# Optimization experiments

Hardware: AMD Instinct MI355X
Metric: run time of the kernel (lower is better)

Reference implementation:

```python
import jax, jax.numpy as jnp
import numpy as np

N_MET = 100_000
N_RXN = 50_000
E_SUB = 2_000_000
E_ALL = 4_000_000
MSG_DIM = 16
HIDDEN = 32


def setup_inputs() -> dict:
    key = jax.random.key(0)
    ks = jax.random.split(key, 16)
    x_met = jax.random.normal(ks[0], (N_MET,), dtype=jnp.float32)
    sto_sub = jax.random.uniform(ks[1], (E_SUB,), dtype=jnp.float32, minval=0.0, maxval=1.0)
    sto_all = jax.random.normal(ks[2], (E_ALL,), dtype=jnp.float32)
    met_sub = jax.random.randint(ks[3], (E_SUB,), 0, N_MET)
    rxn_sub = jax.random.randint(ks[4], (E_SUB,), 0, N_RXN)
    met_all = jax.random.randint(ks[5], (E_ALL,), 0, N_MET)
    rxn_all = jax.random.randint(ks[6], (E_ALL,), 0, N_RXN)
    # msg_mlp: Linear(2->HIDDEN), Tanh, Linear(HIDDEN->MSG_DIM)
    W1m = jax.random.normal(ks[7], (2, HIDDEN), jnp.float32) / np.sqrt(2.0)
    b1m = jnp.zeros((HIDDEN,), jnp.float32)
    W2m = jax.random.normal(ks[8], (HIDDEN, MSG_DIM), jnp.float32) / np.sqrt(HIDDEN)
    b2m = jnp.zeros((MSG_DIM,), jnp.float32)
    # rate_mlp: Linear(MSG_DIM->HIDDEN), Tanh, Linear(HIDDEN->1)
    W1r = jax.random.normal(ks[9], (MSG_DIM, HIDDEN), jnp.float32) / np.sqrt(MSG_DIM)
    b1r = jnp.zeros((HIDDEN,), jnp.float32)
    W2r = jax.random.normal(ks[10], (HIDDEN, 1), jnp.float32) / np.sqrt(HIDDEN)
    b2r = jnp.zeros((1,), jnp.float32)
    return {
        "x_met": x_met, "sto_sub": sto_sub, "sto_all": sto_all,
        "W1m": W1m, "b1m": b1m, "W2m": W2m, "b2m": b2m,
        "W1r": W1r, "b1r": b1r, "W2r": W2r, "b2r": b2r,
        "met_sub": met_sub, "rxn_sub": rxn_sub,
        "met_all": met_all, "rxn_all": rxn_all,
    }


def reference(x_met, sto_sub, sto_all, W1m, b1m, W2m, b2m, W1r, b1r, W2r, b2r,
              met_sub, rxn_sub, met_all, rxn_all):
    # gather substrate node features and build per-edge MLP input [E_sub, 2]
    msg_in = jnp.stack([x_met[met_sub], sto_sub], axis=-1)
    # msg MLP: tanh hidden, linear out -> [E_sub, MSG_DIM]
    msg = jnp.tanh(msg_in @ W1m + b1m) @ W2m + b2m
    # scatter-add messages into reactions -> [N_RXN, MSG_DIM]
    h_rxn = jax.ops.segment_sum(msg, rxn_sub, num_segments=N_RXN)
    # rate MLP + softplus -> per-reaction rate v [N_RXN]
    v = jax.nn.softplus((jnp.tanh(h_rxn @ W1r + b1r) @ W2r + b2r)[:, 0])
    # stoichiometric contributions scattered into metabolites -> dxdt [N_MET]
    contrib = sto_all * v[rxn_all]
    dxdt = jax.ops.segment_sum(contrib, met_all, num_segments=N_MET)
    return dxdt, v
```

## Files before the change

### kernel.cpp

```cpp
#include <hip/hip_runtime.h>

#define N_MET 100000
#define N_RXN 50000
#define E_SUB 2000000
#define E_ALL 4000000
#define MSG_DIM 16
#define HIDDEN 32

#define NBKT_A 391
#define NB_ALL 245
#define TILE_A 16384
#define SLOT_A 12288
#define NBKT_S 782
#define NB_SUB 245
#define TILE_S 8192
#define SLOT_S 4096
#define CHUNK_M 3072


__device__ __forceinline__ float fast_tanh(float x) {
    const float e = __expf(2.0f * x);
    return 1.0f - 2.0f * __builtin_amdgcn_rcpf(e + 1.0f);
}

__global__ __launch_bounds__(1024) void zero_cnt_kernel(
    int* __restrict__ gs, int* __restrict__ ga)
{
    const int t = threadIdx.x;
    for (int i = t; i < NBKT_S; i += 1024) gs[i] = 0;
    for (int i = t; i < NBKT_A; i += 1024) ga[i] = 0;
}


__global__ __launch_bounds__(1024) void scatter_bin_sub_kernel(
    const float* __restrict__ x_met, const float* __restrict__ sto_sub,
    const int* __restrict__ met_sub, const int* __restrict__ rxn_sub,
    int* __restrict__ gcnt, float2* __restrict__ pxs)
{
    __shared__ float2 se[TILE_S];
    __shared__ int cnt[NBKT_S];
    __shared__ int loff[NBKT_S + 1];
    __shared__ int roff[NBKT_S];
    const int t = threadIdx.x, bk = blockIdx.x;
    for (int i = t; i < NBKT_S; i += 1024) cnt[i] = 0;
    __syncthreads();

    const int e0 = bk * TILE_S;
    const int rem = min(TILE_S, E_SUB - e0);
    const int tb = 8 * t;
    float2 pay[8]; int meta[8];
    if (tb + 8 <= rem) {
        const int4 r01 = ((const int4*)(rxn_sub + e0))[2 * t];
        const int4 r23 = ((const int4*)(rxn_sub + e0))[2 * t + 1];
        const int4 m01 = ((const int4*)(met_sub + e0))[2 * t];
        const int4 m23 = ((const int4*)(met_sub + e0))[2 * t + 1];
        const float4 s01 = ((const float4*)(sto_sub + e0))[2 * t];
        const float4 s23 = ((const float4*)(sto_sub + e0))[2 * t + 1];
        const int rr[8] = {r01.x, r01.y, r01.z, r01.w, r23.x, r23.y, r23.z, r23.w};
        const int mm[8] = {m01.x, m01.y, m01.z, m01.w, m23.x, m23.y, m23.z, m23.w};
        const float ss[8] = {s01.x, s01.y, s01.z, s01.w, s23.x, s23.y, s23.z, s23.w};
#pragma unroll
        for (int k = 0; k < 8; ++k) {
            const int r = rr[k];
            const float x = x_met[mm[k]];
            const int sb = (__float_as_int(ss[k]) & ~63) | (r & 63);
            pay[k] = make_float2(x, __int_as_float(sb));
            const int q = r >> 6;
            meta[k] = (atomicAdd(&cnt[q], 1) << 10) | q;
        }
    } else {
#pragma unroll
        for (int k = 0; k < 8; ++k) {
            const int e = e0 + tb + k;
            if (e < E_SUB) {
                const int r = rxn_sub[e];
                const float x = x_met[met_sub[e]];
                const int sb = (__float_as_int(sto_sub[e]) & ~63) | (r & 63);
                pay[k] = make_float2(x, __int_as_float(sb));
                const int q = r >> 6;
                meta[k] = (atomicAdd(&cnt[q], 1) << 10) | q;
            } else meta[k] = -1;
        }
    }
    __syncthreads();

    if (t < 64) {
        int carry = 0;
        for (int bb = 0; bb < NBKT_S; bb += 64) {
            const int idx = bb + t;
            const int val = (idx < NBKT_S) ? cnt[idx] : 0;
            int x = val;
#pragma unroll
            for (int off = 1; off < 64; off <<= 1) {
                const int y = __shfl_up(x, off);
                if (t >= off) x += y;
            }
            if (idx < NBKT_S) loff[idx] = carry + x - val;
            carry += __shfl(x, 63);
        }
        if (t == 0) loff[NBKT_S] = carry;
    }
    __syncthreads();

#pragma unroll
    for (int k = 0; k < 8; ++k) {
        if (meta[k] >= 0)
            se[loff[meta[k] & 1023] + (meta[k] >> 10)] = pay[k];
    }
    for (int q = t; q < NBKT_S; q += 1024) {
        const int len = loff[q + 1] - loff[q];
        roff[q] = len ? atomicAdd(&gcnt[q], len) : 0;
    }
    __syncthreads();

    const int qw = t >> 4, ql = t & 15;
    for (int q = qw; q < NBKT_S; q += 64) {
        const int s = loff[q], len = loff[q + 1] - s;
        float2* d = pxs + (size_t)q * SLOT_S + roff[q];
        for (int i = ql; i < len; i += 16)
            d[i] = se[s + i];
    }
}

__global__ __launch_bounds__(512, 8) void bucket_msg_kernel(
    const float2* __restrict__ pxs, const int* __restrict__ gcnt,
    const float* __restrict__ W1m, const float* __restrict__ b1m,
    const float* __restrict__ W2m, const float* __restrict__ b2m,
    const float* __restrict__ W1r, const float* __restrict__ b1r,
    const float* __restrict__ W2r, const float* __restrict__ b2r,
    float* __restrict__ v)
{
    __shared__ float2 se[CHUNK_M];
    __shared__ float  sth[64 * 33];
    __shared__ int    cnt[64];
    __shared__ int    soff[65];
    __shared__ int    ccnt[64];
    __shared__ float  sW2m[HIDDEN * MSG_DIM];
    __shared__ float  sb2m[MSG_DIM];
    __shared__ float  sW1r[MSG_DIM * HIDDEN];
    __shared__ float  sb1r[HIDDEN];
    __shared__ float  sW2r[HIDDEN];
    __shared__ float  sb2r;
    float* const sh = (float*)se;

    const int t = threadIdx.x;
    const int w = t >> 6, l = t & 63;
    const int half = l >> 5, j = l & 31;

    for (int i = t; i < HIDDEN * MSG_DIM; i += 512) sW2m[i] = W2m[i];
    for (int i = t; i < MSG_DIM * HIDDEN; i += 512) sW1r[i] = W1r[i];
    if (t < MSG_DIM) sb2m[t] = b2m[t];
    if (t < HIDDEN) sb1r[t] = b1r[t];
    if (t >= 64 && t < 64 + HIDDEN) sW2r[t - 64] = W2r[t - 64];
    if (t == 128) sb2r = b2r[0];
    if (t < 64) ccnt[t] = 0;

    const float w1x = W1m[j];
    const float w1y = W1m[HIDDEN + j];
    const float w1b = b1m[j];

    const int b = blockIdx.x;
    const int beg = b * SLOT_S;
    const int end = beg + gcnt[b];

    float acc[4] = {0.0f, 0.0f, 0.0f, 0.0f};

    for (int cb = beg; cb < end; cb += CHUNK_M) {
        if (t < 64) cnt[t] = 0;
        __syncthreads();

        float2 pay[6];
        int meta[6];
#pragma unroll
        for (int k = 0; k < 6; ++k) {
            const int idx = cb + t + (k << 9);
            if (idx < end && t + (k << 9) < CHUNK_M) {
                const float2 pv = pxs[idx];
                const int r = __float_as_int(pv.y) & 63;
                meta[k] = (atomicAdd(&cnt[r], 1) << 6) | r;
                pay[k] = pv;
            } else meta[k] = -1;
        }
        __syncthreads();

        if (t < 64) {
            const int orig = cnt[t];
            int x = orig;
#pragma unroll
            for (int off = 1; off < 64; off <<= 1) {
                const int y = __shfl_up(x, off);
                if (t >= off) x += y;
            }
            soff[t] = x - orig;
            if (t == 63) soff[64] = x;
            ccnt[t] += orig;
        }
        __syncthreads();

#pragma unroll
        for (int k = 0; k < 6; ++k) {
            if (meta[k] >= 0)
                se[soff[meta[k] & 63] + (meta[k] >> 6)] = pay[k];
        }
        __syncthreads();

#pragma unroll
        for (int p = 0; p < 4; ++p) {
            const int q = (w << 3) + (p << 1) + half;
            const int rb = soff[q];
            const int rl = soff[q + 1] - rb;
            float a0 = 0.0f, a1 = 0.0f;
            int i = 0;
            for (; i + 2 <= rl; i += 2) {
                const float2 e0 = se[rb + i];
                const float2 e1 = se[rb + i + 1];
                a0 += fast_tanh(fmaf(e0.x, w1x, fmaf(e0.y, w1y, w1b)));
                a1 += fast_tanh(fmaf(e1.x, w1x, fmaf(e1.y, w1y, w1b)));
            }
            if (i < rl) {
                const float2 e0 = se[rb + i];
                a0 += fast_tanh(fmaf(e0.x, w1x, fmaf(e0.y, w1y, w1b)));
            }
            acc[p] += a0 + a1;
        }
        __syncthreads();
    }

#pragma unroll
    for (int p = 0; p < 4; ++p) {
        const int q = (w << 3) + (p << 1) + half;
        sth[q * 33 + j] = acc[p];
    }
    __syncthreads();

    {
        const int r = t & 63, g = (t >> 6) << 1;
        const float cntf = (float)ccnt[r];
        float h0 = cntf * sb2m[g + 0], h1 = cntf * sb2m[g + 1];
#pragma unroll 8
        for (int jj = 0; jj < HIDDEN; ++jj) {
            const float ts = sth[r * 33 + jj];
            h0 = fmaf(ts, sW2m[jj * MSG_DIM + g + 0], h0);
            h1 = fmaf(ts, sW2m[jj * MSG_DIM + g + 1], h1);
        }
        sh[r * 17 + g + 0] = h0;
        sh[r * 17 + g + 1] = h1;
    }
    __syncthreads();

    if (t < 64) {
        const int r = b * 64 + t;
        if (r < N_RXN) {
            float h[MSG_DIM];
#pragma unroll
            for (int d = 0; d < MSG_DIM; ++d) h[d] = sh[t * 17 + d];
            float acc2 = sb2r;
#pragma unroll 2
            for (int jj = 0; jj < HIDDEN; ++jj) {
                float z = sb1r[jj];
#pragma unroll
                for (int d = 0; d < MSG_DIM; ++d)
                    z = fmaf(h[d], sW1r[d * HIDDEN + jj], z);
                acc2 = fmaf(fast_tanh(z), sW2r[jj], acc2);
            }
            v[r] = fmaxf(acc2, 0.0f) + log1pf(expf(-fabsf(acc2)));
        }
    }
}


__global__ __launch_bounds__(1024) void scatter_bin_kernel(
    const float* __restrict__ sto_all, const float* __restrict__ v,
    const int* __restrict__ met_all, const int* __restrict__ rxn_all,
    int* __restrict__ gcntA, float* __restrict__ pc)
{
    __shared__ float sp[TILE_A];
    __shared__ int cnt[NBKT_A];
    __shared__ int loff[NBKT_A + 1];
    __shared__ int roff[NBKT_A];
    const int t = threadIdx.x, bk = blockIdx.x;
    for (int i = t; i < NBKT_A; i += 1024) cnt[i] = 0;
    __syncthreads();

    const int e0 = bk * TILE_A;
    const int rem = min(TILE_A, E_ALL - e0);
    const int tb = 16 * t;
    int meta[16];
    const bool full = (tb + 16 <= rem);
    if (full) {
#pragma unroll
        for (int kk = 0; kk < 4; ++kk) {
            const int4 m = ((const int4*)(met_all + e0))[4 * t + kk];
            meta[4 * kk + 0] = (atomicAdd(&cnt[m.x >> 8], 1) << 17) | m.x;
            meta[4 * kk + 1] = (atomicAdd(&cnt[m.y >> 8], 1) << 17) | m.y;
            meta[4 * kk + 2] = (atomicAdd(&cnt[m.z >> 8], 1) << 17) | m.z;
            meta[4 * kk + 3] = (atomicAdd(&cnt[m.w >> 8], 1) << 17) | m.w;
        }
    } else {
#pragma unroll
        for (int k = 0; k < 16; ++k) {
            const int e = e0 + tb + k;
            if (e < E_ALL) {
                const int m = met_all[e];
                meta[k] = (atomicAdd(&cnt[m >> 8], 1) << 17) | m;
            } else meta[k] = -1;
        }
    }
    __syncthreads();

    if (t < 64) {
        int carry = 0;
        for (int bb = 0; bb < NBKT_A; bb += 64) {
            const int idx = bb + t;
            const int val = (idx < NBKT_A) ? cnt[idx] : 0;
            int x = val;
#pragma unroll
            for (int off = 1; off < 64; off <<= 1) {
                const int y = __shfl_up(x, off);
                if (t >= off) x += y;
            }
            if (idx < NBKT_A) loff[idx] = carry + x - val;
            carry += __shfl(x, 63);
        }
        if (t == 0) loff[NBKT_A] = carry;
    }
    __syncthreads();

    for (int q = t; q < NBKT_A; q += 1024) {
        const int len = loff[q + 1] - loff[q];
        roff[q] = len ? atomicAdd(&gcntA[q], len) : 0;
    }

    if (full) {
#pragma unroll
        for (int kk = 0; kk < 4; ++kk) {
            const int4 r = ((const int4*)(rxn_all + e0))[4 * t + kk];
            const float4 s = ((const float4*)(sto_all + e0))[4 * t + kk];
            const int rr[4] = {r.x, r.y, r.z, r.w};
            const float ss[4] = {s.x, s.y, s.z, s.w};
#pragma unroll
            for (int u = 0; u < 4; ++u) {
                const int mt = meta[4 * kk + u];
                const int m = mt & 0x1FFFF;
                const float c = ss[u] * v[rr[u]];
                const int cb = (__float_as_int(c) & ~255) | (m & 255);
                sp[loff[m >> 8] + (mt >> 17)] = __int_as_float(cb);
            }
        }
    } else {
#pragma unroll
        for (int k = 0; k < 16; ++k) {
            const int e = e0 + tb + k;
            if (e < E_ALL) {
                const int mt = meta[k];
                const int m = mt & 0x1FFFF;
                const float c = sto_all[e] * v[rxn_all[e]];
                const int cb = (__float_as_int(c) & ~255) | (m & 255);
                sp[loff[m >> 8] + (mt >> 17)] = __int_as_float(cb);
            }
        }
    }
    __syncthreads();

    const int qw = t >> 4, ql = t & 15;
    for (int q = qw; q < NBKT_A; q += 64) {
        const int s = loff[q], len = loff[q + 1] - s;
        float* d = pc + (size_t)q * SLOT_A + roff[q];
        for (int i = ql; i < len; i += 16)
            d[i] = sp[s + i];
    }
}

__global__ __launch_bounds__(512) void bucket_accum_kernel(
    const float* __restrict__ pc, const int* __restrict__ gcntA,
    float* __restrict__ dxdt)
{
    __shared__ float acc[256];
    const int q = blockIdx.x, t = threadIdx.x;
    if (t < 256) acc[t] = 0.0f;
    __syncthreads();
    const float* s = pc + (size_t)q * SLOT_A;
    const int n = gcntA[q];
    const int n4 = n & ~3;
    for (int i = 4 * t; i < n4; i += 2048) {
        const float4 pv = *(const float4*)(s + i);
        atomicAdd(&acc[__float_as_int(pv.x) & 255], pv.x);
        atomicAdd(&acc[__float_as_int(pv.y) & 255], pv.y);
        atomicAdd(&acc[__float_as_int(pv.z) & 255], pv.z);
        atomicAdd(&acc[__float_as_int(pv.w) & 255], pv.w);
    }
    for (int i = n4 + t; i < n; i += 512) {
        const float pv = s[i];
        atomicAdd(&acc[__float_as_int(pv) & 255], pv);
    }
    __syncthreads();
    if (t < 256) {
        const int met = q * 256 + t;
        if (met < N_MET) dxdt[met] = acc[t];
    }
}

extern "C" void kernel_launch(void* const* d_in, const int* in_sizes, int n_in,
                              void* d_out, int out_size, void* d_ws, size_t ws_size,
                              hipStream_t stream) {
    const float* x_met   = (const float*)d_in[0];
    const float* sto_sub = (const float*)d_in[1];
    const float* sto_all = (const float*)d_in[2];
    const float* W1m     = (const float*)d_in[3];
    const float* b1m     = (const float*)d_in[4];
    const float* W2m     = (const float*)d_in[5];
    const float* b2m     = (const float*)d_in[6];
    const float* W1r     = (const float*)d_in[7];
    const float* b1r     = (const float*)d_in[8];
    const float* W2r     = (const float*)d_in[9];
    const float* b2r     = (const float*)d_in[10];
    const int*   met_sub = (const int*)d_in[11];
    const int*   rxn_sub = (const int*)d_in[12];
    const int*   met_all = (const int*)d_in[13];
    const int*   rxn_all = (const int*)d_in[14];

    float* dxdt = (float*)d_out;
    float* v    = dxdt + N_MET;

    char* ws = (char*)d_ws;
    int* gcntS  = (int*)ws;  ws += ((sizeof(int) * NBKT_S + 15) / 16) * 16;
    int* gcntA  = (int*)ws;  ws += ((sizeof(int) * NBKT_A + 15) / 16) * 16;
    char* P = ws;
    float2* pxs = (float2*)P;
    float*  pc  = (float*)P;

    zero_cnt_kernel<<<1, 1024, 0, stream>>>(gcntS, gcntA);

    scatter_bin_sub_kernel<<<NB_SUB, 1024, 0, stream>>>(
        x_met, sto_sub, met_sub, rxn_sub, gcntS, pxs);
    bucket_msg_kernel<<<NBKT_S, 512, 0, stream>>>(
        pxs, gcntS, W1m, b1m, W2m, b2m, W1r, b1r, W2r, b2r, v);

    scatter_bin_kernel<<<NB_ALL, 1024, 0, stream>>>(
        sto_all, v, met_all, rxn_all, gcntA, pc);
    bucket_accum_kernel<<<NBKT_A, 512, 0, stream>>>(pc, gcntA, dxdt);
}
```

Baseline: 233.2 us.

## Balance message-MLP work by splitting sorted edges evenly across half-waves

Each half-wave used to own four fixed reactions and loop over their edges, so load depended on per-reaction edge counts. Now each of 16 half-wave groups takes an equal slice of the sorted chunk and does a segmented reduction, flushing partial tanh sums with shared-memory atomics when the reaction id changes. The tanh also folds the 2*log2(e) factor into the weights so it can use exp2f directly. The cost is extra LDS atomics at segment boundaries and a zeroing pass over the hidden-sum buffer.

```diff
diff --git a/kernel.cpp b/kernel.cpp
--- a/kernel.cpp
+++ b/kernel.cpp
@@ -17,6 +17,13 @@
 #define SLOT_S 4096
 #define CHUNK_M 3072
 
+
+#define TWO_LOG2E 2.8853900817779268f
+
+__device__ __forceinline__ float fast_tanh2(float z2) {
+    const float e = exp2f(z2);
+    return 1.0f - 2.0f * __builtin_amdgcn_rcpf(e + 1.0f);
+}
 
 __device__ __forceinline__ float fast_tanh(float x) {
     const float e = __expf(2.0f * x);
@@ -154,18 +161,18 @@
     if (t >= 64 && t < 64 + HIDDEN) sW2r[t - 64] = W2r[t - 64];
     if (t == 128) sb2r = b2r[0];
     if (t < 64) ccnt[t] = 0;
-
-    const float w1x = W1m[j];
-    const float w1y = W1m[HIDDEN + j];
-    const float w1b = b1m[j];
+    for (int i = t; i < 64 * 33; i += 512) sth[i] = 0.0f;
+
+    const float w1x2 = W1m[j] * TWO_LOG2E;
+    const float w1y2 = W1m[HIDDEN + j] * TWO_LOG2E;
+    const float w1b2 = b1m[j] * TWO_LOG2E;
 
     const int b = blockIdx.x;
     const int beg = b * SLOT_S;
     const int end = beg + gcnt[b];
 
-    float acc[4] = {0.0f, 0.0f, 0.0f, 0.0f};
-
     for (int cb = beg; cb < end; cb += CHUNK_M) {
+        const int clen = min(end - cb, CHUNK_M);
         if (t < 64) cnt[t] = 0;
         __syncthreads();
 
@@ -173,9 +180,9 @@
         int meta[6];
 #pragma unroll
         for (int k = 0; k < 6; ++k) {
-            const int idx = cb + t + (k << 9);
-            if (idx < end && t + (k << 9) < CHUNK_M) {
-                const float2 pv = pxs[idx];
+            const int sl = t + (k << 9);
+            if (sl < clen) {
+                const float2 pv = pxs[cb + sl];
                 const int r = __float_as_int(pv.y) & 63;
                 meta[k] = (atomicAdd(&cnt[r], 1) << 6) | r;
                 pay[k] = pv;
@@ -204,34 +211,26 @@
         }
         __syncthreads();
 
-#pragma unroll
-        for (int p = 0; p < 4; ++p) {
-            const int q = (w << 3) + (p << 1) + half;
-            const int rb = soff[q];
-            const int rl = soff[q + 1] - rb;
-            float a0 = 0.0f, a1 = 0.0f;
-            int i = 0;
-            for (; i + 2 <= rl; i += 2) {
-                const float2 e0 = se[rb + i];
-                const float2 e1 = se[rb + i + 1];
-                a0 += fast_tanh(fmaf(e0.x, w1x, fmaf(e0.y, w1y, w1b)));
-                a1 += fast_tanh(fmaf(e1.x, w1x, fmaf(e1.y, w1y, w1b)));
-            }
-            if (i < rl) {
-                const float2 e0 = se[rb + i];
-                a0 += fast_tanh(fmaf(e0.x, w1x, fmaf(e0.y, w1y, w1b)));
-            }
-            acc[p] += a0 + a1;
+        {
+            const int k16 = (w << 1) + half;
+            const int s0 = (clen * k16) >> 4;
+            const int s1 = (clen * (k16 + 1)) >> 4;
+            int cur = -1;
+            float a = 0.0f;
+#pragma unroll 2
+            for (int i = s0; i < s1; ++i) {
+                const float2 ev = se[i];
+                const int r = __float_as_int(ev.y) & 63;
+                if (r != cur) {
+                    if (cur >= 0) atomicAdd(&sth[cur * 33 + j], a);
+                    cur = r; a = 0.0f;
+                }
+                a += fast_tanh2(fmaf(ev.x, w1x2, fmaf(ev.y, w1y2, w1b2)));
+            }
+            if (cur >= 0) atomicAdd(&sth[cur * 33 + j], a);
         }
         __syncthreads();
     }
-
-#pragma unroll
-    for (int p = 0; p < 4; ++p) {
-        const int q = (w << 3) + (p << 1) + half;
-        sth[q * 33 + j] = acc[p];
-    }
-    __syncthreads();
 
     {
         const int r = t & 63, g = (t >> 6) << 1;
```

After: 240.2 us. +3.0%, slower.

## Bin all-edges by metabolite before rates, gather v in accumulation, merge scatter launches

Applied to the files above, without the earlier changes.

The metabolite-side binning no longer depends on v. It now stores (sto|met-low-bits, rxn index) pairs, and the v gather and multiply move into the accumulation kernel. This lets both scatter passes run in one combined launch, removing a serial dependency and a kernel launch. The cost is twice the bytes per binned edge for the all-edges pass, random gathers of v in the accumulation stage, and a larger workspace, with a fallback path when the workspace is too small.

```diff
diff --git a/kernel.cpp b/kernel.cpp
--- a/kernel.cpp
+++ b/kernel.cpp
@@ -8,8 +8,8 @@
 #define HIDDEN 32
 
 #define NBKT_A 391
-#define NB_ALL 245
-#define TILE_A 16384
+#define NB_ALL 489
+#define TILE_A 8192
 #define SLOT_A 12288
 #define NBKT_S 782
 #define NB_SUB 245
@@ -31,94 +31,179 @@
     for (int i = t; i < NBKT_A; i += 1024) ga[i] = 0;
 }
 
-
-__global__ __launch_bounds__(1024) void scatter_bin_sub_kernel(
+__global__ __launch_bounds__(1024) void scatter_kernel(
     const float* __restrict__ x_met, const float* __restrict__ sto_sub,
     const int* __restrict__ met_sub, const int* __restrict__ rxn_sub,
-    int* __restrict__ gcnt, float2* __restrict__ pxs)
+    const float* __restrict__ sto_all, const int* __restrict__ met_all,
+    const int* __restrict__ rxn_all,
+    int* __restrict__ gcntS, int* __restrict__ gcntA,
+    float2* __restrict__ pxs, float2* __restrict__ pcx, int p2base)
 {
-    __shared__ float2 se[TILE_S];
+    __shared__ float2 se[8192];
     __shared__ int cnt[NBKT_S];
     __shared__ int loff[NBKT_S + 1];
     __shared__ int roff[NBKT_S];
-    const int t = threadIdx.x, bk = blockIdx.x;
-    for (int i = t; i < NBKT_S; i += 1024) cnt[i] = 0;
-    __syncthreads();
-
-    const int e0 = bk * TILE_S;
-    const int rem = min(TILE_S, E_SUB - e0);
-    const int tb = 8 * t;
-    float2 pay[8]; int meta[8];
-    if (tb + 8 <= rem) {
-        const int4 r01 = ((const int4*)(rxn_sub + e0))[2 * t];
-        const int4 r23 = ((const int4*)(rxn_sub + e0))[2 * t + 1];
-        const int4 m01 = ((const int4*)(met_sub + e0))[2 * t];
-        const int4 m23 = ((const int4*)(met_sub + e0))[2 * t + 1];
-        const float4 s01 = ((const float4*)(sto_sub + e0))[2 * t];
-        const float4 s23 = ((const float4*)(sto_sub + e0))[2 * t + 1];
-        const int rr[8] = {r01.x, r01.y, r01.z, r01.w, r23.x, r23.y, r23.z, r23.w};
-        const int mm[8] = {m01.x, m01.y, m01.z, m01.w, m23.x, m23.y, m23.z, m23.w};
-        const float ss[8] = {s01.x, s01.y, s01.z, s01.w, s23.x, s23.y, s23.z, s23.w};
-#pragma unroll
-        for (int k = 0; k < 8; ++k) {
-            const int r = rr[k];
-            const float x = x_met[mm[k]];
-            const int sb = (__float_as_int(ss[k]) & ~63) | (r & 63);
-            pay[k] = make_float2(x, __int_as_float(sb));
-            const int q = r >> 6;
-            meta[k] = (atomicAdd(&cnt[q], 1) << 10) | q;
-        }
-    } else {
-#pragma unroll
-        for (int k = 0; k < 8; ++k) {
-            const int e = e0 + tb + k;
-            if (e < E_SUB) {
-                const int r = rxn_sub[e];
-                const float x = x_met[met_sub[e]];
-                const int sb = (__float_as_int(sto_sub[e]) & ~63) | (r & 63);
+    const int t = threadIdx.x, bk0 = blockIdx.x;
+
+    if (bk0 < p2base) {
+        const int bk = bk0;
+        for (int i = t; i < NBKT_S; i += 1024) cnt[i] = 0;
+        __syncthreads();
+
+        const int e0 = bk * TILE_S;
+        const int rem = min(TILE_S, E_SUB - e0);
+        const int tb = 8 * t;
+        float2 pay[8]; int meta[8];
+        if (tb + 8 <= rem) {
+            const int4 r01 = ((const int4*)(rxn_sub + e0))[2 * t];
+            const int4 r23 = ((const int4*)(rxn_sub + e0))[2 * t + 1];
+            const int4 m01 = ((const int4*)(met_sub + e0))[2 * t];
+            const int4 m23 = ((const int4*)(met_sub + e0))[2 * t + 1];
+            const float4 s01 = ((const float4*)(sto_sub + e0))[2 * t];
+            const float4 s23 = ((const float4*)(sto_sub + e0))[2 * t + 1];
+            const int rr[8] = {r01.x, r01.y, r01.z, r01.w, r23.x, r23.y, r23.z, r23.w};
+            const int mm[8] = {m01.x, m01.y, m01.z, m01.w, m23.x, m23.y, m23.z, m23.w};
+            const float ss[8] = {s01.x, s01.y, s01.z, s01.w, s23.x, s23.y, s23.z, s23.w};
+#pragma unroll
+            for (int k = 0; k < 8; ++k) {
+                const int r = rr[k];
+                const float x = x_met[mm[k]];
+                const int sb = (__float_as_int(ss[k]) & ~63) | (r & 63);
                 pay[k] = make_float2(x, __int_as_float(sb));
                 const int q = r >> 6;
                 meta[k] = (atomicAdd(&cnt[q], 1) << 10) | q;
-            } else meta[k] = -1;
-        }
-    }
-    __syncthreads();
-
-    if (t < 64) {
-        int carry = 0;
-        for (int bb = 0; bb < NBKT_S; bb += 64) {
-            const int idx = bb + t;
-            const int val = (idx < NBKT_S) ? cnt[idx] : 0;
-            int x = val;
-#pragma unroll
-            for (int off = 1; off < 64; off <<= 1) {
-                const int y = __shfl_up(x, off);
-                if (t >= off) x += y;
-            }
-            if (idx < NBKT_S) loff[idx] = carry + x - val;
-            carry += __shfl(x, 63);
-        }
-        if (t == 0) loff[NBKT_S] = carry;
-    }
-    __syncthreads();
-
-#pragma unroll
-    for (int k = 0; k < 8; ++k) {
-        if (meta[k] >= 0)
-            se[loff[meta[k] & 1023] + (meta[k] >> 10)] = pay[k];
-    }
-    for (int q = t; q < NBKT_S; q += 1024) {
-        const int len = loff[q + 1] - loff[q];
-        roff[q] = len ? atomicAdd(&gcnt[q], len) : 0;
-    }
-    __syncthreads();
-
-    const int qw = t >> 4, ql = t & 15;
-    for (int q = qw; q < NBKT_S; q += 64) {
-        const int s = loff[q], len = loff[q + 1] - s;
-        float2* d = pxs + (size_t)q * SLOT_S + roff[q];
-        for (int i = ql; i < len; i += 16)
-            d[i] = se[s + i];
+            }
+        } else {
+#pragma unroll
+            for (int k = 0; k < 8; ++k) {
+                const int e = e0 + tb + k;
+                if (e < E_SUB) {
+                    const int r = rxn_sub[e];
+                    const float x = x_met[met_sub[e]];
+                    const int sb = (__float_as_int(sto_sub[e]) & ~63) | (r & 63);
+                    pay[k] = make_float2(x, __int_as_float(sb));
+                    const int q = r >> 6;
+                    meta[k] = (atomicAdd(&cnt[q], 1) << 10) | q;
+                } else meta[k] = -1;
+            }
+        }
+        __syncthreads();
+
+        if (t < 64) {
+            int carry = 0;
+            for (int bb = 0; bb < NBKT_S; bb += 64) {
+                const int idx = bb + t;
+                const int val = (idx < NBKT_S) ? cnt[idx] : 0;
+                int x = val;
+#pragma unroll
+                for (int off = 1; off < 64; off <<= 1) {
+                    const int y = __shfl_up(x, off);
+                    if (t >= off) x += y;
+                }
+                if (idx < NBKT_S) loff[idx] = carry + x - val;
+                carry += __shfl(x, 63);
+            }
+            if (t == 0) loff[NBKT_S] = carry;
+        }
+        __syncthreads();
+
+#pragma unroll
+        for (int k = 0; k < 8; ++k) {
+            if (meta[k] >= 0)
+                se[loff[meta[k] & 1023] + (meta[k] >> 10)] = pay[k];
+        }
+        for (int q = t; q < NBKT_S; q += 1024) {
+            const int len = loff[q + 1] - loff[q];
+            roff[q] = len ? atomicAdd(&gcntS[q], len) : 0;
+        }
+        __syncthreads();
+
+        const int qw = t >> 4, ql = t & 15;
+        for (int q = qw; q < NBKT_S; q += 64) {
+            const int s = loff[q], len = loff[q + 1] - s;
+            float2* d = pxs + (size_t)q * SLOT_S + roff[q];
+            for (int i = ql; i < len; i += 16)
+                d[i] = se[s + i];
+        }
+    } else {
+        const int bk = bk0 - p2base;
+        for (int i = t; i < NBKT_A; i += 1024) cnt[i] = 0;
+        __syncthreads();
+
+        const int e0 = bk * TILE_A;
+        const int rem = min(TILE_A, E_ALL - e0);
+        const int tb = 8 * t;
+        float2 pay[8]; int meta[8];
+        if (tb + 8 <= rem) {
+            const int4 m01 = ((const int4*)(met_all + e0))[2 * t];
+            const int4 m23 = ((const int4*)(met_all + e0))[2 * t + 1];
+            const int4 r01 = ((const int4*)(rxn_all + e0))[2 * t];
+            const int4 r23 = ((const int4*)(rxn_all + e0))[2 * t + 1];
+            const float4 s01 = ((const float4*)(sto_all + e0))[2 * t];
+            const float4 s23 = ((const float4*)(sto_all + e0))[2 * t + 1];
+            const int mm[8] = {m01.x, m01.y, m01.z, m01.w, m23.x, m23.y, m23.z, m23.w};
+            const int rr[8] = {r01.x, r01.y, r01.z, r01.w, r23.x, r23.y, r23.z, r23.w};
+            const float ss[8] = {s01.x, s01.y, s01.z, s01.w, s23.x, s23.y, s23.z, s23.w};
+#pragma unroll
+            for (int k = 0; k < 8; ++k) {
+                const int m = mm[k];
+                const int sb = (__float_as_int(ss[k]) & ~255) | (m & 255);
+                pay[k] = make_float2(__int_as_float(sb), __int_as_float(rr[k]));
+                const int q = m >> 8;
+                meta[k] = (atomicAdd(&cnt[q], 1) << 9) | q;
+            }
+        } else {
+#pragma unroll
+            for (int k = 0; k < 8; ++k) {
+                const int e = e0 + tb + k;
+                if (e < E_ALL) {
+                    const int m = met_all[e];
+                    const int sb = (__float_as_int(sto_all[e]) & ~255) | (m & 255);
+                    pay[k] = make_float2(__int_as_float(sb),
+                                         __int_as_float(rxn_all[e]));
+                    const int q = m >> 8;
+                    meta[k] = (atomicAdd(&cnt[q], 1) << 9) | q;
+                } else meta[k] = -1;
+            }
+        }
+        __syncthreads();
+
+        if (t < 64) {
+            int carry = 0;
+            for (int bb = 0; bb < NBKT_A; bb += 64) {
+                const int idx = bb + t;
+                const int val = (idx < NBKT_A) ? cnt[idx] : 0;
+                int x = val;
+#pragma unroll
+                for (int off = 1; off < 64; off <<= 1) {
+                    const int y = __shfl_up(x, off);
+                    if (t >= off) x += y;
+                }
+                if (idx < NBKT_A) loff[idx] = carry + x - val;
+                carry += __shfl(x, 63);
+            }
+            if (t == 0) loff[NBKT_A] = carry;
+        }
+        __syncthreads();
+
+#pragma unroll
+        for (int k = 0; k < 8; ++k) {
+            if (meta[k] >= 0)
+                se[loff[meta[k] & 511] + (meta[k] >> 9)] = pay[k];
+        }
+        for (int q = t; q < NBKT_A; q += 1024) {
+            const int len = loff[q + 1] - loff[q];
+            roff[q] = len ? atomicAdd(&gcntA[q], len) : 0;
+        }
+        __syncthreads();
+
+        const int qw = t >> 4, ql = t & 15;
+        for (int q = qw; q < NBKT_A; q += 64) {
+            const int s = loff[q], len = loff[q + 1] - s;
+            float2* d = pcx + (size_t)q * SLOT_A + roff[q];
+            for (int i = ql; i < len; i += 16)
+                d[i] = se[s + i];
+        }
     }
 }
 
@@ -166,6 +251,7 @@
     float acc[4] = {0.0f, 0.0f, 0.0f, 0.0f};
 
     for (int cb = beg; cb < end; cb += CHUNK_M) {
+        const int clen = min(end - cb, CHUNK_M);
         if (t < 64) cnt[t] = 0;
         __syncthreads();
 
@@ -173,9 +259,9 @@
         int meta[6];
 #pragma unroll
         for (int k = 0; k < 6; ++k) {
-            const int idx = cb + t + (k << 9);
-            if (idx < end && t + (k << 9) < CHUNK_M) {
-                const float2 pv = pxs[idx];
+            const int sl = t + (k << 9);
+            if (sl < clen) {
+                const float2 pv = pxs[cb + sl];
                 const int r = __float_as_int(pv.y) & 63;
                 meta[k] = (atomicAdd(&cnt[r], 1) << 6) | r;
                 pay[k] = pv;
@@ -268,130 +354,28 @@
     }
 }
 
-
-__global__ __launch_bounds__(1024) void scatter_bin_kernel(
-    const float* __restrict__ sto_all, const float* __restrict__ v,
-    const int* __restrict__ met_all, const int* __restrict__ rxn_all,
-    int* __restrict__ gcntA, float* __restrict__ pc)
-{
-    __shared__ float sp[TILE_A];
-    __shared__ int cnt[NBKT_A];
-    __shared__ int loff[NBKT_A + 1];
-    __shared__ int roff[NBKT_A];
-    const int t = threadIdx.x, bk = blockIdx.x;
-    for (int i = t; i < NBKT_A; i += 1024) cnt[i] = 0;
-    __syncthreads();
-
-    const int e0 = bk * TILE_A;
-    const int rem = min(TILE_A, E_ALL - e0);
-    const int tb = 16 * t;
-    int meta[16];
-    const bool full = (tb + 16 <= rem);
-    if (full) {
-#pragma unroll
-        for (int kk = 0; kk < 4; ++kk) {
-            const int4 m = ((const int4*)(met_all + e0))[4 * t + kk];
-            meta[4 * kk + 0] = (atomicAdd(&cnt[m.x >> 8], 1) << 17) | m.x;
-            meta[4 * kk + 1] = (atomicAdd(&cnt[m.y >> 8], 1) << 17) | m.y;
-            meta[4 * kk + 2] = (atomicAdd(&cnt[m.z >> 8], 1) << 17) | m.z;
-            meta[4 * kk + 3] = (atomicAdd(&cnt[m.w >> 8], 1) << 17) | m.w;
-        }
-    } else {
-#pragma unroll
-        for (int k = 0; k < 16; ++k) {
-            const int e = e0 + tb + k;
-            if (e < E_ALL) {
-                const int m = met_all[e];
-                meta[k] = (atomicAdd(&cnt[m >> 8], 1) << 17) | m;
-            } else meta[k] = -1;
-        }
-    }
-    __syncthreads();
-
-    if (t < 64) {
-        int carry = 0;
-        for (int bb = 0; bb < NBKT_A; bb += 64) {
-            const int idx = bb + t;
-            const int val = (idx < NBKT_A) ? cnt[idx] : 0;
-            int x = val;
-#pragma unroll
-            for (int off = 1; off < 64; off <<= 1) {
-                const int y = __shfl_up(x, off);
-                if (t >= off) x += y;
-            }
-            if (idx < NBKT_A) loff[idx] = carry + x - val;
-            carry += __shfl(x, 63);
-        }
-        if (t == 0) loff[NBKT_A] = carry;
-    }
-    __syncthreads();
-
-    for (int q = t; q < NBKT_A; q += 1024) {
-        const int len = loff[q + 1] - loff[q];
-        roff[q] = len ? atomicAdd(&gcntA[q], len) : 0;
-    }
-
-    if (full) {
-#pragma unroll
-        for (int kk = 0; kk < 4; ++kk) {
-            const int4 r = ((const int4*)(rxn_all + e0))[4 * t + kk];
-            const float4 s = ((const float4*)(sto_all + e0))[4 * t + kk];
-            const int rr[4] = {r.x, r.y, r.z, r.w};
-            const float ss[4] = {s.x, s.y, s.z, s.w};
-#pragma unroll
-            for (int u = 0; u < 4; ++u) {
-                const int mt = meta[4 * kk + u];
-                const int m = mt & 0x1FFFF;
-                const float c = ss[u] * v[rr[u]];
-                const int cb = (__float_as_int(c) & ~255) | (m & 255);
-                sp[loff[m >> 8] + (mt >> 17)] = __int_as_float(cb);
-            }
-        }
-    } else {
-#pragma unroll
-        for (int k = 0; k < 16; ++k) {
-            const int e = e0 + tb + k;
-            if (e < E_ALL) {
-                const int mt = meta[k];
-                const int m = mt & 0x1FFFF;
-                const float c = sto_all[e] * v[rxn_all[e]];
-                const int cb = (__float_as_int(c) & ~255) | (m & 255);
-                sp[loff[m >> 8] + (mt >> 17)] = __int_as_float(cb);
-            }
-        }
-    }
-    __syncthreads();
-
-    const int qw = t >> 4, ql = t & 15;
-    for (int q = qw; q < NBKT_A; q += 64) {
-        const int s = loff[q], len = loff[q + 1] - s;
-        float* d = pc + (size_t)q * SLOT_A + roff[q];
-        for (int i = ql; i < len; i += 16)
-            d[i] = sp[s + i];
-    }
-}
-
 __global__ __launch_bounds__(512) void bucket_accum_kernel(
-    const float* __restrict__ pc, const int* __restrict__ gcntA,
-    float* __restrict__ dxdt)
+    const float2* __restrict__ pcx, const int* __restrict__ gcntA,
+    const float* __restrict__ v, float* __restrict__ dxdt)
 {
     __shared__ float acc[256];
     const int q = blockIdx.x, t = threadIdx.x;
     if (t < 256) acc[t] = 0.0f;
     __syncthreads();
-    const float* s = pc + (size_t)q * SLOT_A;
+    const float2* s = pcx + (size_t)q * SLOT_A;
     const int n = gcntA[q];
-    const int n4 = n & ~3;
-    for (int i = 4 * t; i < n4; i += 2048) {
+    const int n2 = n & ~1;
+    for (int i = 2 * t; i < n2; i += 1024) {
         const float4 pv = *(const float4*)(s + i);
-        atomicAdd(&acc[__float_as_int(pv.x) & 255], pv.x);
-        atomicAdd(&acc[__float_as_int(pv.y) & 255], pv.y);
-        atomicAdd(&acc[__float_as_int(pv.z) & 255], pv.z);
-        atomicAdd(&acc[__float_as_int(pv.w) & 255], pv.w);
-    }
-    for (int i = n4 + t; i < n; i += 512) {
-        const float pv = s[i];
-        atomicAdd(&acc[__float_as_int(pv) & 255], pv);
+        const float c0 = pv.x * v[__float_as_int(pv.y)];
+        const float c1 = pv.z * v[__float_as_int(pv.w)];
+        atomicAdd(&acc[__float_as_int(pv.x) & 255], c0);
+        atomicAdd(&acc[__float_as_int(pv.z) & 255], c1);
+    }
+    for (int i = n2 + t; i < n; i += 512) {
+        const float2 p = s[i];
+        atomicAdd(&acc[__float_as_int(p.x) & 255],
+                  p.x * v[__float_as_int(p.y)]);
     }
     __syncthreads();
     if (t < 256) {
@@ -422,21 +406,36 @@
     float* dxdt = (float*)d_out;
     float* v    = dxdt + N_MET;
 
+    const size_t PXS_B = (size_t)NBKT_S * SLOT_S * sizeof(float2);
+    const size_t PCX_B = (size_t)NBKT_A * SLOT_A * sizeof(float2);
+
     char* ws = (char*)d_ws;
     int* gcntS  = (int*)ws;  ws += ((sizeof(int) * NBKT_S + 15) / 16) * 16;
     int* gcntA  = (int*)ws;  ws += ((sizeof(int) * NBKT_A + 15) / 16) * 16;
-    char* P = ws;
-    float2* pxs = (float2*)P;
-    float*  pc  = (float*)P;
+    const size_t head = (size_t)(ws - (char*)d_ws);
 
     zero_cnt_kernel<<<1, 1024, 0, stream>>>(gcntS, gcntA);
 
-    scatter_bin_sub_kernel<<<NB_SUB, 1024, 0, stream>>>(
-        x_met, sto_sub, met_sub, rxn_sub, gcntS, pxs);
-    bucket_msg_kernel<<<NBKT_S, 512, 0, stream>>>(
-        pxs, gcntS, W1m, b1m, W2m, b2m, W1r, b1r, W2r, b2r, v);
-
-    scatter_bin_kernel<<<NB_ALL, 1024, 0, stream>>>(
-        sto_all, v, met_all, rxn_all, gcntA, pc);
-    bucket_accum_kernel<<<NBKT_A, 512, 0, stream>>>(pc, gcntA, dxdt);
-}
+    if (ws_size >= head + PXS_B + PCX_B) {
+        float2* pxs = (float2*)ws;
+        float2* pcx = (float2*)(ws + PXS_B);
+        scatter_kernel<<<NB_SUB + NB_ALL, 1024, 0, stream>>>(
+            x_met, sto_sub, met_sub, rxn_sub, sto_all, met_all, rxn_all,
+            gcntS, gcntA, pxs, pcx, NB_SUB);
+        bucket_msg_kernel<<<NBKT_S, 512, 0, stream>>>(
+            pxs, gcntS, W1m, b1m, W2m, b2m, W1r, b1r, W2r, b2r, v);
+        bucket_accum_kernel<<<NBKT_A, 512, 0, stream>>>(pcx, gcntA, v, dxdt);
+    } else {
+        float2* pxs = (float2*)ws;
+        float2* pcx = (float2*)ws;
+        scatter_kernel<<<NB_SUB, 1024, 0, stream>>>(
+            x_met, sto_sub, met_sub, rxn_sub, sto_all, met_all, rxn_all,
+            gcntS, gcntA, pxs, pcx, NB_SUB);
+        bucket_msg_kernel<<<NBKT_S, 512, 0, stream>>>(
+            pxs, gcntS, W1m, b1m, W2m, b2m, W1r, b1r, W2r, b2r, v);
+        scatter_kernel<<<NB_ALL, 1024, 0, stream>>>(
+            x_met, sto_sub, met_sub, rxn_sub, sto_all, met_all, rxn_all,
+            gcntS, gcntA, pxs, pcx, 0);
+        bucket_accum_kernel<<<NBKT_A, 512, 0, stream>>>(pcx, gcntA, v, dxdt);
+    }
+}
```

New measurement: 220.9 us. 1.06x faster.
